# Kernel optimization log

Hardware: AMD Instinct MI355X
Metric: run time of the kernel (lower is better)

## Reference

```python
import jax, jax.numpy as jnp
import numpy as np

N_HEAD = 16
NEG_INF = jnp.float32(-1e30)


def setup_inputs() -> dict:
    key = jax.random.key(0)
    k1, k2, k3 = jax.random.split(key, 3)
    B, T, C = 2, 2048, 1024
    x = jax.random.normal(k1, (B, T, C), dtype=jnp.float32)
    attn_mask = jnp.ones((B, T), dtype=jnp.int32)
    W_qkv = jax.random.normal(k2, (C, 3 * C), dtype=jnp.float32) * (1.0 / np.sqrt(C))
    b_qkv = jnp.zeros((3 * C,), dtype=jnp.float32)
    W_proj = jax.random.normal(k3, (C, C), dtype=jnp.float32) * (1.0 / np.sqrt(C))
    b_proj = jnp.zeros((C,), dtype=jnp.float32)
    return {"x": x, "attn_mask": attn_mask, "W_qkv": W_qkv, "b_qkv": b_qkv,
            "W_proj": W_proj, "b_proj": b_proj}


def reference(x, attn_mask, W_qkv, b_qkv, W_proj, b_proj):
    B, T, C = x.shape
    H = N_HEAD
    hd = C // H
    qkv = x @ W_qkv + b_qkv                       # [B,T,3C]
    q, k, v = jnp.split(qkv, 3, axis=-1)
    q = q.reshape(B, T, H, hd).transpose(0, 2, 1, 3)  # [B,H,T,hd]
    k = k.reshape(B, T, H, hd).transpose(0, 2, 1, 3)
    v = v.reshape(B, T, H, hd).transpose(0, 2, 1, 3)
    att = jnp.einsum('bhqd,bhkd->bhqk', q, k) / jnp.float32(np.sqrt(hd))  # [B,H,T,T]
    causal = jnp.tril(jnp.ones((T, T), dtype=bool))[None, None]           # [1,1,T,T]
    pad = (attn_mask != 0)[:, None, None, :]                              # [B,1,1,T]
    att = jnp.where(causal & pad, att, NEG_INF)
    att = jax.nn.softmax(att, axis=-1)
    y = jnp.einsum('bhqk,bhkd->bhqd', att, v)     # [B,H,T,hd]
    y = y.transpose(0, 2, 1, 3).reshape(B, T, C)
    return y @ W_proj + b_proj
```

## Files before the change

### kernel.cpp

```cpp
#include <hip/hip_runtime.h>

#define T_SEQ 2048
#define NHEAD 16
#define HD 64
#define CDIM 1024

typedef __bf16 bf16x8 __attribute__((ext_vector_type(8)));
typedef float f32x4 __attribute__((ext_vector_type(4)));
typedef float f32x16 __attribute__((ext_vector_type(16)));

union U16x8 { uint4 u4; unsigned short s[8]; bf16x8 b; };

__device__ __forceinline__ float bf2f(unsigned short u) {
    return __uint_as_float(((unsigned int)u) << 16);
}
__device__ __forceinline__ unsigned short f2bf(float f) {
    unsigned int u = __float_as_uint(f);
    u += 0x7fffu + ((u >> 16) & 1u);
    return (unsigned short)(u >> 16);
}
__device__ __forceinline__ unsigned short f2bf_fast(float f) {
    return (unsigned short)((__float_as_uint(f) + 0x8000u) >> 16);
}
__device__ __forceinline__ U16x8 load8f(const float* __restrict__ p) {
    U16x8 r;
    float4 f0 = *(const float4*)p;
    float4 f1 = *(const float4*)(p + 4);
    r.s[0] = f2bf(f0.x); r.s[1] = f2bf(f0.y); r.s[2] = f2bf(f0.z); r.s[3] = f2bf(f0.w);
    r.s[4] = f2bf(f1.x); r.s[5] = f2bf(f1.y); r.s[6] = f2bf(f1.z); r.s[7] = f2bf(f1.w);
    return r;
}

__device__ __forceinline__ void async_copy16(const unsigned short* g, unsigned short* l) {
    __builtin_amdgcn_global_load_lds(
        (const __attribute__((address_space(1))) unsigned int*)g,
        (__attribute__((address_space(3))) unsigned int*)l, 16, 0, 0);
}

#define LOG2E 1.442695040f

#define BAR()    asm volatile("s_barrier" ::: "memory")
#define LGKM0()  asm volatile("s_waitcnt lgkmcnt(0)" ::: "memory")
#define VMC6()   asm volatile("s_waitcnt vmcnt(6)" ::: "memory")
#define VMC0()   asm volatile("s_waitcnt vmcnt(0)" ::: "memory")

__device__ __forceinline__ unsigned int cvtpk_bf16(float lo, float hi) {
    unsigned int r;
    asm("v_cvt_pk_bf16_f32 %0, %1, %2" : "=v"(r) : "v"(lo), "v"(hi));
    return r;
}
__device__ __forceinline__ void plane32swap(unsigned int &x, unsigned int &y) {
    asm("v_permlane32_swap_b32 %0, %1" : "+v"(x), "+v"(y));
}

__device__ __forceinline__ void transpose_tile(
    const float* __restrict__ in, unsigned short* __restrict__ out,
    int R, int C, int r0, int c0, float tile[64][65])
{
    const int tid = threadIdx.x;
    const int rr = tid >> 4;
    const int cc = (tid & 15) * 4;
#pragma unroll
    for (int p = 0; p < 4; ++p) {
        float4 v = *(const float4*)&in[(size_t)(r0 + p * 16 + rr) * C + c0 + cc];
        tile[p * 16 + rr][cc] = v.x;
        tile[p * 16 + rr][cc + 1] = v.y;
        tile[p * 16 + rr][cc + 2] = v.z;
        tile[p * 16 + rr][cc + 3] = v.w;
    }
    __syncthreads();
    const int n = tid >> 2;
    const int s = (tid & 3) * 8;
#pragma unroll
    for (int p = 0; p < 2; ++p) {
        const int k = s + p * 32;
        U16x8 o;
#pragma unroll
        for (int j = 0; j < 8; ++j) o.s[j] = f2bf(tile[k + j][n]);
        *(uint4*)&out[(size_t)(c0 + n) * R + r0 + k] = o.u4;
    }
}

__global__ __launch_bounds__(256) void prep(
    const float* __restrict__ X,     unsigned short* __restrict__ Xb,
    const float* __restrict__ Wqkv,  unsigned short* __restrict__ Wqkvt,
    const float* __restrict__ Wproj, unsigned short* __restrict__ Wprojt)
{
    __shared__ float tile[64][65];
    const int bid = blockIdx.x;
    if (bid < 2048) {
        const int i = (bid * 256 + threadIdx.x) * 8;
        U16x8 o = load8f(&X[i]);
        *(uint4*)&Xb[i] = o.u4;
    } else if (bid < 2816) {
        const int u = bid - 2048;
        transpose_tile(Wqkv, Wqkvt, CDIM, 3 * CDIM, (u & 15) * 64, (u >> 4) * 64, tile);
    } else {
        const int u = bid - 2816;
        transpose_tile(Wproj, Wprojt, CDIM, CDIM, (u & 15) * 64, (u >> 4) * 64, tile);
    }
}

__device__ __forceinline__ void gemm128_core(
    const unsigned short* __restrict__ A,
    const unsigned short* __restrict__ Bt,
    int K, int m0, int n0,
    unsigned short* As, unsigned short* Bs, f32x4 acc[4][4])
{
    const int tid = threadIdx.x;
    const int w = tid >> 6, lane = tid & 63;
    const int ln = lane & 15, quad = lane >> 4;
    const int wm = w >> 1, wn = w & 1;
    const int lr = lane >> 3;
    const int lc = (lane & 7) * 8;

    for (int kb = 0; kb < K; kb += 64) {
        __syncthreads();
#pragma unroll
        for (int i = 0; i < 4; ++i) {
            async_copy16(&A[(size_t)(m0 + w * 32 + i * 8 + lr) * K + kb + lc],
                         &As[(w * 32 + i * 8) * 64]);
            async_copy16(&Bt[(size_t)(n0 + w * 32 + i * 8 + lr) * K + kb + lc],
                         &Bs[(w * 32 + i * 8) * 64]);
        }
        __syncthreads();
#pragma unroll
        for (int kk = 0; kk < 2; ++kk) {
            U16x8 af[4], bff[4];
#pragma unroll
            for (int i = 0; i < 4; ++i)
                af[i].u4 = *(const uint4*)&As[(wm * 64 + i * 16 + ln) * 64 + kk * 32 + quad * 8];
#pragma unroll
            for (int j = 0; j < 4; ++j)
                bff[j].u4 = *(const uint4*)&Bs[(wn * 64 + j * 16 + ln) * 64 + kk * 32 + quad * 8];
#pragma unroll
            for (int i = 0; i < 4; ++i)
#pragma unroll
                for (int j = 0; j < 4; ++j)
                    acc[i][j] = __builtin_amdgcn_mfma_f32_16x16x32_bf16(af[i].b, bff[j].b, acc[i][j], 0, 0, 0);
        }
    }
}

__device__ __forceinline__ void stageA(const unsigned short* __restrict__ A,
                                       unsigned short* buf,
                                       int m0, int t, int unit, int w, int lane)
{
#pragma unroll
    for (int s = 0; s < 2; ++s) {
        const int r0 = s * 128 + unit * 64 + w * 8;
        const int row = r0 + (lane >> 3);
        const int col = (16 * (lane & 7)) ^ ((row & 4) ? 32 : 0);
        const unsigned short* src = A + (size_t)(m0 + row) * CDIM + t * 64 + (col >> 1);
        async_copy16(src, buf + r0 * 64);
    }
}

__device__ __forceinline__ void stageB(const unsigned short* __restrict__ B,
                                       unsigned short* buf,
                                       int n0, int t, int unit, int w, int lane)
{
#pragma unroll
    for (int s = 0; s < 2; ++s) {
        const int slice = s * 8 + w;
        const int r0 = (slice >> 2) * 64 + unit * 32 + (slice & 3) * 8;
        const int row = r0 + (lane >> 3);
        const int col = (16 * (lane & 7)) ^ ((row & 4) ? 32 : 0);
        const unsigned short* src = B + (size_t)(n0 + row) * CDIM + t * 64 + (col >> 1);
        async_copy16(src, buf + r0 * 64);
    }
}

__device__ __forceinline__ void readA(U16x8 af[4][2], const unsigned short* buf,
                                      int wm, int qm, int ln, int quad)
{
#pragma unroll
    for (int i = 0; i < 4; ++i) {
        const int row = wm * 128 + qm * 64 + i * 16 + ln;
        const int sw = (row & 4) ? 32 : 0;
#pragma unroll
        for (int kk = 0; kk < 2; ++kk) {
            const int byt = row * 128 + ((kk * 64 + quad * 16) ^ sw);
            af[i][kk].u4 = *(const uint4*)((const char*)buf + byt);
        }
    }
}

__device__ __forceinline__ void readB(U16x8 bf[2][2], const unsigned short* buf,
                                      int wn, int qn, int ln, int quad)
{
#pragma unroll
    for (int jj = 0; jj < 2; ++jj) {
        const int row = wn * 64 + qn * 32 + jj * 16 + ln;
        const int sw = (row & 4) ? 32 : 0;
#pragma unroll
        for (int kk = 0; kk < 2; ++kk) {
            const int byt = row * 128 + ((kk * 64 + quad * 16) ^ sw);
            bf[jj][kk].u4 = *(const uint4*)((const char*)buf + byt);
        }
    }
}

template<int QM, int QN>
__device__ __forceinline__ void mfma16(f32x4 acc[8][4], const U16x8 af[4][2],
                                       const U16x8 bf[2][2])
{
    __builtin_amdgcn_s_setprio(1);
#pragma unroll
    for (int i = 0; i < 4; ++i)
#pragma unroll
        for (int jj = 0; jj < 2; ++jj)
#pragma unroll
            for (int kk = 0; kk < 2; ++kk)
                acc[QM * 4 + i][QN * 2 + jj] = __builtin_amdgcn_mfma_f32_16x16x32_bf16(
                    af[i][kk].b, bf[jj][kk].b, acc[QM * 4 + i][QN * 2 + jj], 0, 0, 0);
    __builtin_amdgcn_s_setprio(0);
}

__global__ __launch_bounds__(512) void qkv8(
    const unsigned short* __restrict__ Xb,
    const unsigned short* __restrict__ Wt,
    const float* __restrict__ bias,
    unsigned short* __restrict__ Qp,
    unsigned short* __restrict__ Kp,
    unsigned short* __restrict__ Vtp)
{
    __shared__ __align__(1024) unsigned short smem[4][16384];
    unsigned short* Ab0 = smem[0];
    unsigned short* Ab1 = smem[1];
    unsigned short* Bb0 = smem[2];
    unsigned short* Bb1 = smem[3];

    const int tid = threadIdx.x;
    const int w = tid >> 6, lane = tid & 63;
    const int ln = lane & 15, quad = lane >> 4;
    const int wm = w >> 2, wn = w & 3;

    const int bid = blockIdx.x;
    const int swz = (bid & 7) * 24 + (bid >> 3);
    const int nt = swz % 12, mt = swz / 12;
    const int m0 = mt * 256, n0 = nt * 256;

    f32x4 acc[8][4];
#pragma unroll
    for (int i = 0; i < 8; ++i)
#pragma unroll
        for (int j = 0; j < 4; ++j) acc[i][j] = (f32x4){0.f, 0.f, 0.f, 0.f};

    stageA(Xb, Ab0, m0, 0, 0, w, lane);
    stageB(Wt, Bb0, n0, 0, 0, w, lane);
    stageB(Wt, Bb0, n0, 0, 1, w, lane);
    stageA(Xb, Ab0, m0, 0, 1, w, lane);
    stageA(Xb, Ab1, m0, 1, 0, w, lane);
    stageB(Wt, Bb1, n0, 1, 0, w, lane);
    stageB(Wt, Bb1, n0, 1, 1, w, lane);
    VMC6();
    BAR();

    U16x8 af[4][2], bq0[2][2], bq1[2][2];

    for (int j = 0; j < 7; ++j) {
        const int e = 2 * j, o = 2 * j + 1;
        readA(af, Ab0, wm, 0, ln, quad);
        readB(bq0, Bb0, wn, 0, ln, quad);
        stageA(Xb, Ab1, m0, o, 1, w, lane);
        BAR(); LGKM0();
        mfma16<0, 0>(acc, af, bq0);
        LGKM0(); BAR();
        readB(bq1, Bb0, wn, 1, ln, quad);
        stageA(Xb, Ab0, m0, e + 2, 0, w, lane);
        BAR(); LGKM0();
        mfma16<0, 1>(acc, af, bq1);
        LGKM0(); BAR();
        readA(af, Ab0, wm, 1, ln, quad);
        stageB(Wt, Bb0, n0, e + 2, 0, w, lane);
        BAR(); LGKM0();
        mfma16<1, 0>(acc, af, bq0);
        LGKM0(); BAR();
        stageB(Wt, Bb0, n0, e + 2, 1, w, lane);
        BAR();
        mfma16<1, 1>(acc, af, bq1);
        VMC6(); BAR();
        readA(af, Ab1, wm, 0, ln, quad);
        readB(bq0, Bb1, wn, 0, ln, quad);
        stageA(Xb, Ab0, m0, e + 2, 1, w, lane);
        BAR(); LGKM0();
        mfma16<0, 0>(acc, af, bq0);
        LGKM0(); BAR();
        readB(bq1, Bb1, wn, 1, ln, quad);
        stageA(Xb, Ab1, m0, o + 2, 0, w, lane);
        BAR(); LGKM0();
        mfma16<0, 1>(acc, af, bq1);
        LGKM0(); BAR();
        readA(af, Ab1, wm, 1, ln, quad);
        stageB(Wt, Bb1, n0, o + 2, 0, w, lane);
        BAR(); LGKM0();
        mfma16<1, 0>(acc, af, bq0);
        LGKM0(); BAR();
        stageB(Wt, Bb1, n0, o + 2, 1, w, lane);
        BAR();
        mfma16<1, 1>(acc, af, bq1);
        VMC6(); BAR();
    }

    stageA(Xb, Ab1, m0, 15, 1, w, lane);
    VMC0(); BAR();

    readA(af, Ab0, wm, 0, ln, quad);
    readB(bq0, Bb0, wn, 0, ln, quad);
    readB(bq1, Bb0, wn, 1, ln, quad);
    mfma16<0, 0>(acc, af, bq0);
    mfma16<0, 1>(acc, af, bq1);
    readA(af, Ab0, wm, 1, ln, quad);
    mfma16<1, 0>(acc, af, bq0);
    mfma16<1, 1>(acc, af, bq1);

    readA(af, Ab1, wm, 0, ln, quad);
    readB(bq0, Bb1, wn, 0, ln, quad);
    readB(bq1, Bb1, wn, 1, ln, quad);
    mfma16<0, 0>(acc, af, bq0);
    mfma16<0, 1>(acc, af, bq1);
    readA(af, Ab1, wm, 1, ln, quad);
    mfma16<1, 0>(acc, af, bq0);
    mfma16<1, 1>(acc, af, bq1);

    const int which = n0 >> 10;
    float bv[4];
#pragma unroll
    for (int jj = 0; jj < 4; ++jj) bv[jj] = bias[n0 + wn * 64 + jj * 16 + ln];

    if (which < 2) {
        unsigned short* dst = (which == 0) ? Qp : Kp;
#pragma unroll
        for (int jj = 0; jj < 4; ++jj) {
            const int n = n0 + wn * 64 + jj * 16 + ln;
            const int h = (n >> 6) & 15, d = n & 63;
#pragma unroll
            for (int i = 0; i < 8; ++i)
#pragma unroll
                for (int r = 0; r < 4; ++r) {
                    const int m = m0 + wm * 128 + i * 16 + quad * 4 + r;
                    const int b = m >> 11, tt = m & 2047;
                    dst[(((size_t)(b * NHEAD + h) * T_SEQ) + tt) * HD + d] =
                        f2bf(acc[i][jj][r] + bv[jj]);
                }
        }
    } else {
#pragma unroll
        for (int jj = 0; jj < 4; ++jj) {
            const int n = n0 + wn * 64 + jj * 16 + ln;
            const int c = n - 2048;
#pragma unroll
            for (int i = 0; i < 8; ++i) {
                const int m00 = m0 + wm * 128 + i * 16 + quad * 4;
                const int b = m00 >> 11, tt = m00 & 2047;
                ushort4 pk;
                pk.x = f2bf(acc[i][jj][0] + bv[jj]);
                pk.y = f2bf(acc[i][jj][1] + bv[jj]);
                pk.z = f2bf(acc[i][jj][2] + bv[jj]);
                pk.w = f2bf(acc[i][jj][3] + bv[jj]);
                *(ushort4*)&Vtp[(size_t)(b * 1024 + c) * T_SEQ + tt] = pk;
            }
        }
    }
}

__global__ __launch_bounds__(256) void proj_gemm(
    const unsigned short* __restrict__ Yin,
    const unsigned short* __restrict__ Wt,
    const float* __restrict__ bias,
    float* __restrict__ out)
{
    __shared__ unsigned short As[128 * 64];
    __shared__ unsigned short Bs[128 * 64];
    const int m0 = blockIdx.y * 128;
    const int n0 = blockIdx.x * 128;

    f32x4 acc[4][4];
#pragma unroll
    for (int i = 0; i < 4; ++i)
#pragma unroll
        for (int j = 0; j < 4; ++j) acc[i][j] = (f32x4){0.f, 0.f, 0.f, 0.f};

    gemm128_core(Yin, Wt, CDIM, m0, n0, As, Bs, acc);

    const int tid = threadIdx.x;
    const int w = tid >> 6, lane = tid & 63;
    const int ln = lane & 15, quad = lane >> 4;
    const int wm = w >> 1, wn = w & 1;

#pragma unroll
    for (int j = 0; j < 4; ++j) {
        const int n = n0 + wn * 64 + j * 16 + ln;
        const float bv = bias[n];
#pragma unroll
        for (int i = 0; i < 4; ++i)
#pragma unroll
            for (int r = 0; r < 4; ++r) {
                const int m = m0 + wm * 64 + i * 16 + quad * 4 + r;
                out[(size_t)m * CDIM + n] = acc[i][j][r] + bv;
            }
    }
}


__device__ __forceinline__ int swz(int row, int slot) {
    return row * 64 + ((slot ^ (row & 7)) << 3);
}

__global__ __launch_bounds__(256) void flash_attn32(
    const unsigned short* __restrict__ Qp,
    const unsigned short* __restrict__ Kp,
    const unsigned short* __restrict__ Vtp,
    const int* __restrict__ mask,
    unsigned short* __restrict__ Y)
{
    __shared__ unsigned short Ks[64 * 64];
    __shared__ unsigned short Vs[64 * 64];
    __shared__ float mask_arr[64];
    __shared__ float als[4][32];
    __shared__ int flagu;

    const int bh = blockIdx.x;
    const int qb = 15 - blockIdx.y;
    const int b = bh >> 4, h = bh & 15;
    const int tid = threadIdx.x;
    const int w = tid >> 6, lane = tid & 63;
    const int l31 = lane & 31, hi = lane >> 5;
    const int row8 = tid >> 3, seg = tid & 7;
    const size_t base = (size_t)bh * T_SEQ * HD;
    const int qB = qb * 128;
    const int qw0 = qB + w * 32;
    const int qv = qw0 + l31;
    const int jlast = 2 * qb + 1;

    U16x8 qf[4];
    {
        const unsigned short* qrow = &Qp[base + (size_t)qv * HD];
#pragma unroll
        for (int c = 0; c < 4; ++c)
            qf[c].u4 = *(const uint4*)&qrow[c * 16 + hi * 8];
    }

    f32x16 oA0, oA1;
#pragma unroll
    for (int r = 0; r < 16; ++r) { oA0[r] = 0.f; oA1[r] = 0.f; }
    float m_r = -3.0e38f, mL = 0.f, l_r = 0.f;

    uint4 kr0, kr1, vr0, vr1;
    float mf = 0.f;
    {
        const unsigned short* kp0 = &Kp[base + (size_t)row8 * HD + seg * 8];
        kr0 = *(const uint4*)kp0;
        kr1 = *(const uint4*)(kp0 + 32 * HD);
        const unsigned short* vp0 = &Vtp[base + (size_t)row8 * T_SEQ + seg * 8];
        vr0 = *(const uint4*)vp0;
        vr1 = *(const uint4*)(vp0 + 32 * T_SEQ);
        if (tid < 64) mf = mask[b * T_SEQ + tid] ? 0.f : -1.0e30f;
    }

    for (int j = 0; j <= jlast; ++j) {
        __syncthreads();
        *(uint4*)&Ks[swz(row8, seg)]      = kr0;
        *(uint4*)&Ks[swz(row8 + 32, seg)] = kr1;
        *(uint4*)&Vs[swz(row8, seg)]      = vr0;
        *(uint4*)&Vs[swz(row8 + 32, seg)] = vr1;
        if (w == 0) {
            const int k = lane;
            const int idx = ((k >> 2) & 1) * 32 + (k >> 5) * 16 + ((k & 31) >> 3) * 4 + (k & 3);
            mask_arr[idx] = mf;
            const unsigned long long bb = __ballot(mf == 0.f);
            if (lane == 0) flagu = (bb == 0xFFFFFFFFFFFFFFFFull) ? 0 : 1;
        }
        __syncthreads();

        if (j < jlast) {
            const unsigned short* kp0 = &Kp[base + (size_t)((j + 1) * 64 + row8) * HD + seg * 8];
            kr0 = *(const uint4*)kp0;
            kr1 = *(const uint4*)(kp0 + 32 * HD);
            const unsigned short* vp0 = &Vtp[base + (size_t)row8 * T_SEQ + (j + 1) * 64 + seg * 8];
            vr0 = *(const uint4*)vp0;
            vr1 = *(const uint4*)(vp0 + 32 * T_SEQ);
            if (tid < 64) mf = mask[b * T_SEQ + (j + 1) * 64 + tid] ? 0.f : -1.0e30f;
        }

        const bool skipw = (j * 64 > qw0 + 31);
        if (!skipw) {
            const bool edge = (j * 64 + 63 > qw0);
            const int anymask = flagu;

            f32x16 sc0, sc1;
#pragma unroll
            for (int r = 0; r < 16; ++r) { sc0[r] = 0.f; sc1[r] = 0.f; }
#pragma unroll
            for (int c = 0; c < 4; ++c) {
                U16x8 ka0, ka1;
                const int r0 = l31, r1 = 32 + l31;
                ka0.u4 = *(const uint4*)&Ks[r0 * 64 + (((2 * c + hi) ^ (r0 & 7)) << 3)];
                ka1.u4 = *(const uint4*)&Ks[r1 * 64 + (((2 * c + hi) ^ (r1 & 7)) << 3)];
                sc0 = __builtin_amdgcn_mfma_f32_32x32x16_bf16(ka0.b, qf[c].b, sc0, 0, 0, 0);
                sc1 = __builtin_amdgcn_mfma_f32_32x32x16_bf16(ka1.b, qf[c].b, sc1, 0, 0, 0);
            }

            if (anymask) {
#pragma unroll
                for (int g = 0; g < 4; ++g) {
                    const f32x4 m0v = *(const f32x4*)&mask_arr[hi * 32 + g * 4];
                    const f32x4 m1v = *(const f32x4*)&mask_arr[hi * 32 + 16 + g * 4];
#pragma unroll
                    for (int t = 0; t < 4; ++t) {
                        sc0[g * 4 + t] = fmaf(sc0[g * 4 + t], 0.125f, m0v[t]);
                        sc1[g * 4 + t] = fmaf(sc1[g * 4 + t], 0.125f, m1v[t]);
                    }
                }
            } else {
#pragma unroll
                for (int r = 0; r < 16; ++r) {
                    sc0[r] *= 0.125f;
                    sc1[r] *= 0.125f;
                }
            }
            if (edge) {
#pragma unroll
                for (int r = 0; r < 16; ++r) {
                    const int krow = (r & 3) + 8 * (r >> 2) + 4 * hi;
                    if (j * 64 + krow > qv)      sc0[r] = -1.0e30f;
                    if (j * 64 + 32 + krow > qv) sc1[r] = -1.0e30f;
                }
            }

            float tm = -3.0e38f;
#pragma unroll
            for (int r = 0; r < 16; ++r)
                tm = fmaxf(tm, fmaxf(sc0[r], sc1[r]));
            tm = fmaxf(tm, __shfl_xor(tm, 32));

            if (__any(tm > m_r + 8.f)) {
                const float mn = fmaxf(m_r, tm);
                const float a = __builtin_amdgcn_exp2f((m_r - mn) * LOG2E);
                m_r = mn; mL = mn * LOG2E;
                l_r *= a;
                if (hi == 0) als[w][l31] = a;
                f32x4 av[4];
#pragma unroll
                for (int g = 0; g < 4; ++g)
                    av[g] = *(const f32x4*)&als[w][g * 8 + hi * 4];
#pragma unroll
                for (int r = 0; r < 16; ++r) {
                    const float aa = av[r >> 2][r & 3];
                    oA0[r] *= aa; oA1[r] *= aa;
                }
            }

            float ps = 0.f;
#pragma unroll
            for (int r = 0; r < 16; ++r) {
                const float p0 = __builtin_amdgcn_exp2f(fmaf(sc0[r], LOG2E, -mL));
                const float p1 = __builtin_amdgcn_exp2f(fmaf(sc1[r], LOG2E, -mL));
                sc0[r] = p0; sc1[r] = p1;
                ps += p0 + p1;
            }
            l_r += ps;

#pragma unroll
            for (int c = 0; c < 4; ++c) {
                const int rb = (c & 1) * 8;
                unsigned int x0, y0, x1, y1;
                if (c < 2) {
                    x0 = cvtpk_bf16(sc0[rb + 0], sc0[rb + 1]);
                    y0 = cvtpk_bf16(sc0[rb + 4], sc0[rb + 5]);
                    x1 = cvtpk_bf16(sc0[rb + 2], sc0[rb + 3]);
                    y1 = cvtpk_bf16(sc0[rb + 6], sc0[rb + 7]);
                } else {
                    x0 = cvtpk_bf16(sc1[rb + 0], sc1[rb + 1]);
                    y0 = cvtpk_bf16(sc1[rb + 4], sc1[rb + 5]);
                    x1 = cvtpk_bf16(sc1[rb + 2], sc1[rb + 3]);
                    y1 = cvtpk_bf16(sc1[rb + 6], sc1[rb + 7]);
                }
                plane32swap(x0, y0);
                plane32swap(x1, y1);
                U16x8 pa;
                pa.u4 = make_uint4(x0, x1, y0, y1);
                {
                    const int vr_0 = l31, vr_1 = 32 + l31;
                    U16x8 vb0, vb1;
                    vb0.u4 = *(const uint4*)&Vs[vr_0 * 64 + (((2 * c + hi) ^ (vr_0 & 7)) << 3)];
                    vb1.u4 = *(const uint4*)&Vs[vr_1 * 64 + (((2 * c + hi) ^ (vr_1 & 7)) << 3)];
                    oA0 = __builtin_amdgcn_mfma_f32_32x32x16_bf16(pa.b, vb0.b, oA0, 0, 0, 0);
                    oA1 = __builtin_amdgcn_mfma_f32_32x32x16_bf16(pa.b, vb1.b, oA1, 0, 0, 0);
                }
            }
        }
    }

    const float lt = l_r + __shfl_xor(l_r, 32);
    if (hi == 0) als[w][l31] = 1.0f / lt;
    f32x4 lv[4];
#pragma unroll
    for (int g = 0; g < 4; ++g)
        lv[g] = *(const f32x4*)&als[w][g * 8 + hi * 4];

#pragma unroll
    for (int r = 0; r < 16; ++r) {
        const int q = qw0 + (r & 3) + 8 * (r >> 2) + 4 * hi;
        const float sl = lv[r >> 2][r & 3];
        const size_t row = (size_t)(b * T_SEQ + q);
        Y[row * CDIM + h * HD + l31]      = f2bf(oA0[r] * sl);
        Y[row * CDIM + h * HD + 32 + l31] = f2bf(oA1[r] * sl);
    }
}

extern "C" void kernel_launch(void* const* d_in, const int* in_sizes, int n_in,
                              void* d_out, int out_size, void* d_ws, size_t ws_size,
                              hipStream_t stream)
{
    const float* X     = (const float*)d_in[0];
    const int*   mask  = (const int*)d_in[1];
    const float* Wqkv  = (const float*)d_in[2];
    const float* bqkv  = (const float*)d_in[3];
    const float* Wproj = (const float*)d_in[4];
    const float* bproj = (const float*)d_in[5];
    float* out = (float*)d_out;

    const size_t per = (size_t)2 * NHEAD * T_SEQ * HD;
    unsigned short* Qp     = (unsigned short*)d_ws;
    unsigned short* Kp     = Qp + per;
    unsigned short* Vtp    = Kp + per;
    unsigned short* Xb     = Vtp + per;
    unsigned short* Yp     = Xb;
    unsigned short* Wqkvt  = Xb + per;
    unsigned short* Wprojt = Wqkvt + (size_t)3 * CDIM * CDIM;

    prep<<<3072, 256, 0, stream>>>(X, Xb, Wqkv, Wqkvt, Wproj, Wprojt);
    qkv8<<<192, 512, 0, stream>>>(Xb, Wqkvt, bqkv, Qp, Kp, Vtp);
    flash_attn32<<<dim3(2 * NHEAD, 16), 256, 0, stream>>>(Qp, Kp, Vtp, mask, Yp);
    proj_gemm<<<dim3(8, 32), 256, 0, stream>>>(Yp, Wprojt, bproj, out);
}
```

Baseline: 215.3 us.

## Split KV loop for long causal query blocks and merge partials

```diff
diff --git a/kernel.cpp b/kernel.cpp
--- a/kernel.cpp
+++ b/kernel.cpp
@@ -18,9 +18,6 @@
     unsigned int u = __float_as_uint(f);
     u += 0x7fffu + ((u >> 16) & 1u);
     return (unsigned short)(u >> 16);
-}
-__device__ __forceinline__ unsigned short f2bf_fast(float f) {
-    return (unsigned short)((__float_as_uint(f) + 0x8000u) >> 16);
 }
 __device__ __forceinline__ U16x8 load8f(const float* __restrict__ p) {
     U16x8 r;
@@ -413,7 +410,10 @@
     const unsigned short* __restrict__ Kp,
     const unsigned short* __restrict__ Vtp,
     const int* __restrict__ mask,
-    unsigned short* __restrict__ Y)
+    unsigned short* __restrict__ Y,
+    unsigned short* __restrict__ Po,
+    float* __restrict__ Pm,
+    float* __restrict__ Pl)
 {
     __shared__ unsigned short Ks[64 * 64];
     __shared__ unsigned short Vs[64 * 64];
@@ -422,7 +422,13 @@
     __shared__ int flagu;
 
     const int bh = blockIdx.x;
-    const int qb = 15 - blockIdx.y;
+    const int y = blockIdx.y;
+    int qb, j0, jstep;
+    bool split;
+    if (y < 16) { qb = 15 - (y >> 1); j0 = y & 1; jstep = 2; split = true; }
+    else        { qb = 23 - y;        j0 = 0;     jstep = 1; split = false; }
+    const int sgk = y & 1;
+
     const int b = bh >> 4, h = bh & 15;
     const int tid = threadIdx.x;
     const int w = tid >> 6, lane = tid & 63;
@@ -450,16 +456,16 @@
     uint4 kr0, kr1, vr0, vr1;
     float mf = 0.f;
     {
-        const unsigned short* kp0 = &Kp[base + (size_t)row8 * HD + seg * 8];
+        const unsigned short* kp0 = &Kp[base + (size_t)(j0 * 64 + row8) * HD + seg * 8];
         kr0 = *(const uint4*)kp0;
         kr1 = *(const uint4*)(kp0 + 32 * HD);
-        const unsigned short* vp0 = &Vtp[base + (size_t)row8 * T_SEQ + seg * 8];
+        const unsigned short* vp0 = &Vtp[base + (size_t)row8 * T_SEQ + j0 * 64 + seg * 8];
         vr0 = *(const uint4*)vp0;
         vr1 = *(const uint4*)(vp0 + 32 * T_SEQ);
-        if (tid < 64) mf = mask[b * T_SEQ + tid] ? 0.f : -1.0e30f;
-    }
-
-    for (int j = 0; j <= jlast; ++j) {
+        if (tid < 64) mf = mask[b * T_SEQ + j0 * 64 + tid] ? 0.f : -1.0e30f;
+    }
+
+    for (int j = j0; j <= jlast; j += jstep) {
         __syncthreads();
         *(uint4*)&Ks[swz(row8, seg)]      = kr0;
         *(uint4*)&Ks[swz(row8 + 32, seg)] = kr1;
@@ -474,14 +480,15 @@
         }
         __syncthreads();
 
-        if (j < jlast) {
-            const unsigned short* kp0 = &Kp[base + (size_t)((j + 1) * 64 + row8) * HD + seg * 8];
+        const int jn = j + jstep;
+        if (jn <= jlast) {
+            const unsigned short* kp0 = &Kp[base + (size_t)(jn * 64 + row8) * HD + seg * 8];
             kr0 = *(const uint4*)kp0;
             kr1 = *(const uint4*)(kp0 + 32 * HD);
-            const unsigned short* vp0 = &Vtp[base + (size_t)row8 * T_SEQ + (j + 1) * 64 + seg * 8];
+            const unsigned short* vp0 = &Vtp[base + (size_t)row8 * T_SEQ + jn * 64 + seg * 8];
             vr0 = *(const uint4*)vp0;
             vr1 = *(const uint4*)(vp0 + 32 * T_SEQ);
-            if (tid < 64) mf = mask[b * T_SEQ + (j + 1) * 64 + tid] ? 0.f : -1.0e30f;
+            if (tid < 64) mf = mask[b * T_SEQ + jn * 64 + tid] ? 0.f : -1.0e30f;
         }
 
         const bool skipw = (j * 64 > qw0 + 31);
@@ -594,20 +601,67 @@
     }
 
     const float lt = l_r + __shfl_xor(l_r, 32);
-    if (hi == 0) als[w][l31] = 1.0f / lt;
-    f32x4 lv[4];
-#pragma unroll
-    for (int g = 0; g < 4; ++g)
-        lv[g] = *(const f32x4*)&als[w][g * 8 + hi * 4];
-
-#pragma unroll
-    for (int r = 0; r < 16; ++r) {
-        const int q = qw0 + (r & 3) + 8 * (r >> 2) + 4 * hi;
-        const float sl = lv[r >> 2][r & 3];
-        const size_t row = (size_t)(b * T_SEQ + q);
-        Y[row * CDIM + h * HD + l31]      = f2bf(oA0[r] * sl);
-        Y[row * CDIM + h * HD + 32 + l31] = f2bf(oA1[r] * sl);
-    }
+
+    if (split) {
+        const int pidx = (bh * 8 + (qb - 8)) * 2 + sgk;
+        if (hi == 0) {
+            Pm[pidx * 128 + w * 32 + l31] = m_r;
+            Pl[pidx * 128 + w * 32 + l31] = lt;
+        }
+#pragma unroll
+        for (int r = 0; r < 16; ++r) {
+            const int qlc = w * 32 + (r & 3) + 8 * (r >> 2) + 4 * hi;
+            Po[(size_t)pidx * 8192 + qlc * 64 + l31]      = f2bf(oA0[r]);
+            Po[(size_t)pidx * 8192 + qlc * 64 + 32 + l31] = f2bf(oA1[r]);
+        }
+    } else {
+        if (hi == 0) als[w][l31] = 1.0f / lt;
+        f32x4 lv[4];
+#pragma unroll
+        for (int g = 0; g < 4; ++g)
+            lv[g] = *(const f32x4*)&als[w][g * 8 + hi * 4];
+#pragma unroll
+        for (int r = 0; r < 16; ++r) {
+            const int q = qw0 + (r & 3) + 8 * (r >> 2) + 4 * hi;
+            const float sl = lv[r >> 2][r & 3];
+            const size_t row = (size_t)(b * T_SEQ + q);
+            Y[row * CDIM + h * HD + l31]      = f2bf(oA0[r] * sl);
+            Y[row * CDIM + h * HD + 32 + l31] = f2bf(oA1[r] * sl);
+        }
+    }
+}
+
+__global__ __launch_bounds__(256) void merge_attn(
+    const unsigned short* __restrict__ Po,
+    const float* __restrict__ Pm, const float* __restrict__ Pl,
+    unsigned short* __restrict__ Y)
+{
+    const int u = blockIdx.x;
+    const int bh = u & 31;
+    const int v = u >> 5;
+    const int qc = v >> 2, part = v & 3;
+    const int tid = threadIdx.x;
+    const int ql = part * 32 + (tid >> 3);
+    const int d0 = (tid & 7) * 8;
+    const int b = bh >> 4, h = bh & 15;
+    const int i0 = (bh * 8 + qc) * 2, i1 = i0 + 1;
+
+    const float m0 = Pm[i0 * 128 + ql], m1 = Pm[i1 * 128 + ql];
+    const float l0 = Pl[i0 * 128 + ql], l1 = Pl[i1 * 128 + ql];
+    const float M = fmaxf(m0, m1);
+    const float f0 = __builtin_amdgcn_exp2f((m0 - M) * LOG2E);
+    const float f1 = __builtin_amdgcn_exp2f((m1 - M) * LOG2E);
+    const float inv = 1.0f / (f0 * l0 + f1 * l1);
+
+    U16x8 a, c, o;
+    a.u4 = *(const uint4*)&Po[(size_t)i0 * 8192 + ql * 64 + d0];
+    c.u4 = *(const uint4*)&Po[(size_t)i1 * 8192 + ql * 64 + d0];
+#pragma unroll
+    for (int j = 0; j < 8; ++j)
+        o.s[j] = f2bf((f0 * bf2f(a.s[j]) + f1 * bf2f(c.s[j])) * inv);
+
+    const int q = 1024 + qc * 128 + ql;
+    *(uint4*)&Y[(size_t)(b * T_SEQ + q) * CDIM + h * HD + d0] = o.u4;
 }
 
 extern "C" void kernel_launch(void* const* d_in, const int* in_sizes, int n_in,
@@ -630,9 +684,13 @@
     unsigned short* Yp     = Xb;
     unsigned short* Wqkvt  = Xb + per;
     unsigned short* Wprojt = Wqkvt + (size_t)3 * CDIM * CDIM;
+    unsigned short* Po     = Wprojt + (size_t)CDIM * CDIM;
+    float*          Pm     = (float*)(Po + (size_t)512 * 8192);
+    float*          Pl     = Pm + 512 * 128;
 
     prep<<<3072, 256, 0, stream>>>(X, Xb, Wqkv, Wqkvt, Wproj, Wprojt);
     qkv8<<<192, 512, 0, stream>>>(Xb, Wqkvt, bqkv, Qp, Kp, Vtp);
-    flash_attn32<<<dim3(2 * NHEAD, 16), 256, 0, stream>>>(Qp, Kp, Vtp, mask, Yp);
+    flash_attn32<<<dim3(2 * NHEAD, 24), 256, 0, stream>>>(Qp, Kp, Vtp, mask, Yp, Po, Pm, Pl);
+    merge_attn<<<1024, 256, 0, stream>>>(Po, Pm, Pl, Yp);
     proj_gemm<<<dim3(8, 32), 256, 0, stream>>>(Yp, Wprojt, bproj, out);
 }
```

Measured after the change: 213.8 us. Within noise of the previous version (-0.7%).
